# Kernel optimization log

Measured on AMD Instinct MI355X. Metric: run time of the kernel, lower is better.

Reference implementation:

```python
import jax, jax.numpy as jnp
import numpy as np

B, N, D_IN, D_OUT, H, W = 2, 2048, 1024, 1024, 16, 64
DH = D_OUT // H


def setup_inputs() -> dict:
    key = jax.random.key(0)
    ks = jax.random.split(key, 6)
    x = jax.random.normal(ks[0], (B, N, D_IN), dtype=jnp.float32)
    s_in = 1.0 / np.sqrt(D_IN)
    s_out = 1.0 / np.sqrt(D_OUT)
    wq = jax.random.normal(ks[1], (D_IN, D_OUT), dtype=jnp.float32) * s_in
    wk = jax.random.normal(ks[2], (D_IN, D_OUT), dtype=jnp.float32) * s_in
    wv = jax.random.normal(ks[3], (D_IN, D_OUT), dtype=jnp.float32) * s_in
    wo = jax.random.normal(ks[4], (D_OUT, D_OUT), dtype=jnp.float32) * s_out
    # sparse global tokens: every 256th token is global
    global_attention = (jnp.arange(N)[None, :] % 256 == 0) & jnp.ones((B, 1), bool)
    return {"x": x, "wq": wq, "wk": wk, "wv": wv, "wo": wo,
            "global_attention": global_attention}


def _mask(global_attention):
    # True = masked out. Causal local window + global rows/cols unmasked.
    i = jnp.arange(N)[:, None]
    j = jnp.arange(N)[None, :]
    allowed = (i - j < W) & (i >= j)          # causal sliding window
    local_mask = ~allowed                      # [N, N], True = masked
    g = global_attention                       # [B, N] bool
    # global token j clears row j and column j of the mask
    global_clear = g[:, :, None] | g[:, None, :]   # [B, N, N]
    return local_mask[None, :, :] & ~global_clear  # [B, N, N]


def reference(x, wq, wk, wv, wo, global_attention):
    b, n, _ = x.shape
    q = (x @ wq).reshape(b, n, H, DH).transpose(0, 2, 1, 3)  # [b,h,n,dh]
    k = (x @ wk).reshape(b, n, H, DH).transpose(0, 2, 1, 3)
    v = (x @ wv).reshape(b, n, H, DH).transpose(0, 2, 1, 3)
    scores = jnp.einsum('bhqd,bhkd->bhqk', q, k) / jnp.sqrt(jnp.float32(DH))
    mask = _mask(global_attention)[:, None, :, :]            # [b,1,n,n]
    scores = jnp.where(mask, -jnp.inf, scores)
    attn = jax.nn.softmax(scores, axis=-1)
    ctx = jnp.einsum('bhqk,bhkd->bqhd', attn, v).reshape(b, n, D_OUT)
    return ctx @ wo
```

## Files before the change

kernel.cpp:

```cpp
#include <hip/hip_runtime.h>


using u16 = unsigned short;
using u32 = unsigned int;

typedef __attribute__((ext_vector_type(8))) short bf16x8;
typedef __attribute__((ext_vector_type(4))) float f32x4;

__device__ __forceinline__ float b2f(u16 s) {
  union { u32 u; float f; } x; x.u = ((u32)s) << 16; return x.f;
}
__device__ __forceinline__ u16 f2b(float f) {
  union { float f; u32 u; } x; x.f = f;
  u32 r = (x.u + 0x7fffu + ((x.u >> 16) & 1u)) >> 16;
  return (u16)r;
}

__global__ __launch_bounds__(256) void k_pre(const float* __restrict__ x,
                                             u16* __restrict__ xb,
                                             const float* __restrict__ wq,
                                             const float* __restrict__ wk,
                                             const float* __restrict__ wv,
                                             const float* __restrict__ wo,
                                             u16* __restrict__ wqkvT,
                                             u16* __restrict__ woT) {
  __shared__ float tile[64][65];
  const int bid = blockIdx.x;
  if (bid < 2048) {
    int idx = (bid * 256 + threadIdx.x) * 8;
    float4 a = *(const float4*)(x + idx);
    float4 b = *(const float4*)(x + idx + 4);
    uint4 o;
    o.x = (u32)f2b(a.x) | ((u32)f2b(a.y) << 16);
    o.y = (u32)f2b(a.z) | ((u32)f2b(a.w) << 16);
    o.z = (u32)f2b(b.x) | ((u32)f2b(b.y) << 16);
    o.w = (u32)f2b(b.z) | ((u32)f2b(b.w) << 16);
    *(uint4*)(xb + idx) = o;
  } else {
    const int id = bid - 2048;
    const int z = id >> 8, xy = id & 255;
    const float* src = (z == 0) ? wq : (z == 1) ? wk : (z == 2) ? wv : wo;
    u16* dst = (z < 3) ? (wqkvT + ((size_t)z << 20)) : woT;
    const int n0 = (xy & 15) * 64, k0 = (xy >> 4) * 64;
    const int tx = threadIdx.x & 63, ty = threadIdx.x >> 6;
    #pragma unroll
    for (int r = 0; r < 64; r += 4)
      tile[r + ty][tx] = src[(size_t)(k0 + r + ty) * 1024 + n0 + tx];
    __syncthreads();
    #pragma unroll
    for (int r = 0; r < 64; r += 4)
      dst[(size_t)(n0 + r + ty) * 1024 + k0 + tx] = f2b(tile[tx][r + ty]);
  }
}

__device__ __forceinline__ void gload16(const u16* g, u16* l) {
  __builtin_amdgcn_global_load_lds((const __attribute__((address_space(1))) void*)g,
                                   (__attribute__((address_space(3))) void*)l, 16, 0, 0);
}

__global__ __launch_bounds__(512, 4) void k_qkv(const u16* __restrict__ A,
                                                const u16* __restrict__ Bt,
                                                u16* __restrict__ C) {
  __shared__ __attribute__((aligned(16))) u16 lds[40960];
  const int K = 1024, N = 3072, NT = 16;
  const int t = threadIdx.x;
  const int wid = t >> 6, lane = t & 63;
  const int l4 = lane >> 4, l16 = lane & 15;
  const int qr = wid >> 1, qc = wid & 1;
  const int d = blockIdx.y * gridDim.x + blockIdx.x;
  const int qq = (gridDim.x * gridDim.y) >> 3;
  const int tau = (d & 7) * qq + (d >> 3);
  const int bn = tau % gridDim.x, bm = tau / gridDim.x;
  const u16* Ab = A + (size_t)bm * 128 * K;
  const u16* Bb = Bt + (size_t)bn * 192 * K;
  const int rowbase = wid * 8 + (lane >> 3);
  const int qcg = rowbase >> 5, rrb = rowbase & 31;
  const int scc = ((lane & 7) ^ ((lane >> 3) & 7)) << 3;
  const int rsw = (l16 & 7);
  f32x4 acc[3][2][2] = {};
  bf16x8 af[2][2], bf[2][2];

  #define STG_A(BUF, KT)                                                           \
    { u16* lb = lds + (BUF) * 8192 + (wid << 9);                                   \
      _Pragma("unroll")                                                            \
      for (int i = 0; i < 2; ++i)                                                  \
        gload16(Ab + (size_t)(i * 64 + rowbase) * K + (KT) * 64 + scc,             \
                lb + i * 4096); }

  #define STG_B1(BUF, KT, I)                                                       \
    { u16* lb = lds + 16384 + (BUF) * 12288 + (I) * 4096 + (wid << 9);             \
      gload16(Bb + (size_t)(qcg * 96 + (I) * 32 + rrb) * K + (KT) * 64 + scc, lb); }

  #define LOAD_A(AS)                                                               \
    { _Pragma("unroll")                                                            \
      for (int m = 0; m < 2; ++m) {                                                \
        const int ro = qr * 32 + m * 16 + l16;                                     \
        _Pragma("unroll")                                                          \
        for (int ks = 0; ks < 2; ++ks)                                             \
          af[m][ks] = *(const bf16x8*)&(AS)[ro * 64 + (((ks * 4 + l4) ^ rsw) << 3)]; \
      } }

  #define LOAD_B(BS, NH)                                                           \
    { _Pragma("unroll")                                                            \
      for (int n = 0; n < 2; ++n) {                                                \
        const int po = (NH) * 64 + qc * 32 + n * 16 + l16;                         \
        _Pragma("unroll")                                                          \
        for (int ks = 0; ks < 2; ++ks)                                             \
          bf[n][ks] = *(const bf16x8*)&(BS)[po * 64 + (((ks * 4 + l4) ^ rsw) << 3)]; \
      } }

  #define QUAD(NH)                                                                 \
    { __builtin_amdgcn_s_setprio(1);                                               \
      _Pragma("unroll")                                                            \
      for (int m = 0; m < 2; ++m)                                                  \
        _Pragma("unroll")                                                          \
        for (int n = 0; n < 2; ++n) {                                              \
          f32x4 c = acc[NH][m][n];                                                 \
          c = __builtin_amdgcn_mfma_f32_16x16x32_bf16(af[m][0], bf[n][0], c, 0, 0, 0); \
          c = __builtin_amdgcn_mfma_f32_16x16x32_bf16(af[m][1], bf[n][1], c, 0, 0, 0); \
          acc[NH][m][n] = c;                                                       \
        }                                                                          \
      __builtin_amdgcn_s_setprio(0); }

  STG_A(0, 0);
  STG_B1(0, 0, 0); STG_B1(0, 0, 1); STG_B1(0, 0, 2);
  STG_A(1, 1);
  STG_B1(1, 1, 0);
  asm volatile("s_waitcnt vmcnt(3)" ::: "memory");
  __builtin_amdgcn_s_barrier();

  for (int tt = 0; tt < NT; ++tt) {
    const int beta = tt & 1;
    const u16* As = lds + beta * 8192;
    const u16* Bs = lds + 16384 + beta * 12288;
    LOAD_A(As);
    LOAD_B(Bs, 0);
    if (tt + 1 < NT) STG_B1(beta ^ 1, tt + 1, 1);
    __builtin_amdgcn_s_barrier();
    QUAD(0);
    __builtin_amdgcn_s_barrier();
    LOAD_B(Bs, 1);
    if (tt + 1 < NT) STG_B1(beta ^ 1, tt + 1, 2);
    __builtin_amdgcn_s_barrier();
    QUAD(1);
    __builtin_amdgcn_s_barrier();
    LOAD_B(Bs, 2);
    if (tt + 2 < NT) {
      STG_A(beta, tt + 2);
      STG_B1(beta, tt + 2, 0);
    }
    __builtin_amdgcn_s_barrier();
    QUAD(2);
    if (tt + 2 < NT)      asm volatile("s_waitcnt vmcnt(3)" ::: "memory");
    else if (tt + 1 < NT) asm volatile("s_waitcnt vmcnt(0)" ::: "memory");
    __builtin_amdgcn_s_barrier();
  }
  #undef STG_A
  #undef STG_B1
  #undef LOAD_A
  #undef LOAD_B
  #undef QUAD

  #pragma unroll
  for (int nh = 0; nh < 3; ++nh)
    #pragma unroll
    for (int m = 0; m < 2; ++m) {
      const int row0 = bm * 128 + qr * 32 + m * 16 + l4 * 4;
      #pragma unroll
      for (int n = 0; n < 2; ++n) {
        const int col = bn * 192 + qc * 96 + nh * 32 + n * 16 + l16;
        #pragma unroll
        for (int r = 0; r < 4; ++r)
          C[(size_t)(row0 + r) * N + col] = f2b(acc[nh][m][n][r]);
      }
    }
}

__global__ __launch_bounds__(512, 2) void k_out(const u16* __restrict__ A,
                                                const u16* __restrict__ Bt,
                                                float* __restrict__ C,
                                                const float* __restrict__ gpart,
                                                u16* __restrict__ ctxw) {
  __shared__ __attribute__((aligned(16))) u16 lds[32768];
  const int K = 1024, N = 1024, NT = 16;
  const int t = threadIdx.x;
  const int wid = t >> 6, lane = t & 63;
  const int l4 = lane >> 4, l16 = lane & 15;
  const int qr = wid >> 2, qc = wid & 3;
  const int d = blockIdx.y * gridDim.x + blockIdx.x;
  const int qq = (gridDim.x * gridDim.y) >> 3;
  const int tau = (d & 7) * qq + (d >> 3);
  const int bn = tau % gridDim.x, bm = tau / gridDim.x;
  const u16* Ab = A + (size_t)bm * 128 * K;
  const u16* Bb = Bt + (size_t)bn * 128 * K;
  const int rowbase = wid * 8 + (lane >> 3);
  const int qcg = rowbase >> 4, rrb = rowbase & 15;
  const int scc = ((lane & 7) ^ ((lane >> 3) & 7)) << 3;
  const int rsw = (l16 & 7);
  f32x4 acc[2][4] = {};
  bf16x8 af[4][2], bf[2][2];

  if ((bm & 1) == 0) {
    if (t < 256) {
      const int bb = bm >> 4;
      const int irow = (bm & 15) * 128;
      const int row8 = (bm & 15) >> 1;
      const int h = t >> 4;
      const int d0 = (t & 15) * 4;
      const float* g0 = gpart + ((size_t)(bb * 16 + h) * 32) * 520;
      float o0 = 0.f, o1 = 0.f, o2 = 0.f, o3 = 0.f, ls = 0.f;
      for (int q = 0; q < 32; ++q) {
        const float4 v = *(const float4*)(g0 + q * 520 + row8 * 64 + d0);
        o0 += v.x; o1 += v.y; o2 += v.z; o3 += v.w;
        ls += g0[q * 520 + 512 + row8];
      }
      const float inv = 1.f / ls;
      u16* cw = ctxw + ((size_t)(bb * 2048 + irow)) * 1024 + h * 64 + d0;
      cw[0] = f2b(o0 * inv); cw[1] = f2b(o1 * inv);
      cw[2] = f2b(o2 * inv); cw[3] = f2b(o3 * inv);
    }
    __syncthreads();
  }

  #define OSTG_A(BUF, KT)                                                          \
    { u16* lb = lds + (BUF) * 8192 + (wid << 9);                                   \
      _Pragma("unroll")                                                            \
      for (int i = 0; i < 2; ++i)                                                  \
        gload16(Ab + (size_t)(i * 64 + rowbase) * K + (KT) * 64 + scc,             \
                lb + i * 4096); }

  #define OSTG_B(BUF, KT)                                                          \
    { u16* lb = lds + 16384 + (BUF) * 8192 + (wid << 9);                           \
      _Pragma("unroll")                                                            \
      for (int nf = 0; nf < 2; ++nf)                                               \
        gload16(Bb + (size_t)(qcg * 32 + nf * 16 + rrb) * K + (KT) * 64 + scc,     \
                lb + nf * 4096); }

  #define OLOAD()                                                                  \
    { _Pragma("unroll")                                                            \
      for (int m = 0; m < 4; ++m) {                                                \
        const int ro = qr * 64 + m * 16 + l16;                                     \
        _Pragma("unroll")                                                          \
        for (int ks = 0; ks < 2; ++ks)                                             \
          af[m][ks] = *(const bf16x8*)&As[ro * 64 + (((ks * 4 + l4) ^ rsw) << 3)]; \
      }                                                                            \
      _Pragma("unroll")                                                            \
      for (int nf = 0; nf < 2; ++nf) {                                             \
        const int po = nf * 64 + qc * 16 + l16;                                    \
        _Pragma("unroll")                                                          \
        for (int ks = 0; ks < 2; ++ks)                                             \
          bf[nf][ks] = *(const bf16x8*)&Bs[po * 64 + (((ks * 4 + l4) ^ rsw) << 3)]; \
      } }

  OSTG_A(0, 0); OSTG_B(0, 0);
  OSTG_A(1, 1); OSTG_B(1, 1);
  asm volatile("s_waitcnt vmcnt(4)" ::: "memory");
  __builtin_amdgcn_s_barrier();

  for (int tt = 0; tt < NT; ++tt) {
    const int beta = tt & 1;
    const u16* As = lds + beta * 8192;
    const u16* Bs = lds + 16384 + beta * 8192;
    OLOAD();
    asm volatile("s_waitcnt lgkmcnt(0)" ::: "memory");
    __builtin_amdgcn_s_barrier();
    if (tt + 2 < NT) { OSTG_A(beta, tt + 2); OSTG_B(beta, tt + 2); }
    __builtin_amdgcn_s_setprio(1);
    #pragma unroll
    for (int nf = 0; nf < 2; ++nf)
      #pragma unroll
      for (int m = 0; m < 4; ++m) {
        f32x4 c = acc[nf][m];
        c = __builtin_amdgcn_mfma_f32_16x16x32_bf16(af[m][0], bf[nf][0], c, 0, 0, 0);
        c = __builtin_amdgcn_mfma_f32_16x16x32_bf16(af[m][1], bf[nf][1], c, 0, 0, 0);
        acc[nf][m] = c;
      }
    __builtin_amdgcn_s_setprio(0);
    if (tt + 2 < NT)      asm volatile("s_waitcnt vmcnt(4)" ::: "memory");
    else if (tt + 1 < NT) asm volatile("s_waitcnt vmcnt(0)" ::: "memory");
    __builtin_amdgcn_s_barrier();
  }
  #undef OSTG_A
  #undef OSTG_B
  #undef OLOAD

  #pragma unroll
  for (int nf = 0; nf < 2; ++nf)
    #pragma unroll
    for (int m = 0; m < 4; ++m) {
      const int row0 = bm * 128 + qr * 64 + m * 16 + l4 * 4;
      const int col = bn * 128 + qc * 32 + nf * 16 + l16;
      #pragma unroll
      for (int r = 0; r < 4; ++r)
        C[(size_t)(row0 + r) * N + col] = acc[nf][m][r];
    }
}

__global__ __launch_bounds__(256) void k_attn_tile(const u16* __restrict__ qkv,
                                                   u16* __restrict__ ctx,
                                                   float* __restrict__ gpart) {
  __shared__ u16 buf[26880];
  __shared__ u16 Qgs[16 * 72];
  __shared__ u16 Pgs[16 * 72];
  __shared__ float lred[4][16];
  u16* Qs = buf;
  u16* Ks = buf + 4608;
  u16* Vt = buf + 16128;
  u16* Ps = buf;

  const int t = threadIdx.x, wid = t >> 6, lane = t & 63;
  const int l4 = lane >> 4, l16 = lane & 15;
  const int qt = blockIdx.x, h = blockIdx.y, b = blockIdx.z;
  const int q0 = qt * 64;
  const int kbase = q0 - 64;
  const size_t base = (size_t)b * 2048 * 3072;
  const u16* Qg = qkv + base + h * 64;
  const u16* Kg = qkv + base + 1024 + h * 64;
  const u16* Vg = qkv + base + 2048 + h * 64;

  const int rA = t >> 3;
  const int cA = (t & 7) * 8;

  uint4 qv0 = *(const uint4*)&Qg[(size_t)(q0 + rA) * 3072 + cA];
  uint4 qv1 = *(const uint4*)&Qg[(size_t)(q0 + rA + 32) * 3072 + cA];
  uint4 qgv;
  if (t < 64) qgv = *(const uint4*)&Qg[(size_t)(rA * 256) * 3072 + cA];
  uint4 kv0 = *(const uint4*)&Kg[(size_t)max(kbase + rA, 0) * 3072 + cA];
  uint4 kv1 = *(const uint4*)&Kg[(size_t)max(kbase + rA + 32, 0) * 3072 + cA];
  uint4 kv2 = *(const uint4*)&Kg[(size_t)max(kbase + rA + 64, 0) * 3072 + cA];
  uint4 kv3 = *(const uint4*)&Kg[(size_t)max(kbase + rA + 96, 0) * 3072 + cA];
  uint4 kv4;
  if (t < 64) kv4 = *(const uint4*)&Kg[(size_t)(rA * 256) * 3072 + cA];
  uint4 vv0 = *(const uint4*)&Vg[(size_t)max(kbase + rA, 0) * 3072 + cA];
  uint4 vv1 = *(const uint4*)&Vg[(size_t)max(kbase + rA + 32, 0) * 3072 + cA];
  uint4 vv2 = *(const uint4*)&Vg[(size_t)max(kbase + rA + 64, 0) * 3072 + cA];
  uint4 vv3 = *(const uint4*)&Vg[(size_t)max(kbase + rA + 96, 0) * 3072 + cA];
  uint4 vv4;
  if (t < 64) vv4 = *(const uint4*)&Vg[(size_t)(rA * 256) * 3072 + cA];

  for (int z = t; z < 64 * 24; z += 256) {
    int dd = z / 24, j = 136 + z % 24;
    Vt[dd * 168 + j] = 0;
  }
  if (t >= 64 && t < 128) {
    uint4 zz = {0, 0, 0, 0};
    *(uint4*)&Qgs[rA * 72 + cA] = zz;
  }

  *(uint4*)&Qs[rA * 72 + cA] = qv0;
  *(uint4*)&Qs[(rA + 32) * 72 + cA] = qv1;
  if (t < 64) *(uint4*)&Qgs[rA * 72 + cA] = qgv;
  *(uint4*)&Ks[rA * 72 + cA] = kv0;
  *(uint4*)&Ks[(rA + 32) * 72 + cA] = kv1;
  *(uint4*)&Ks[(rA + 64) * 72 + cA] = kv2;
  *(uint4*)&Ks[(rA + 96) * 72 + cA] = kv3;
  if (t < 64) *(uint4*)&Ks[(rA + 128) * 72 + cA] = kv4;

  #define VW1(DD, VAL, CH_, R7_)                                                   \
    { const int kd_ = (((DD) >> 3) ^ (DD)) & 7;                                    \
      const int chs_ = ((CH_) < 16) ? ((CH_) ^ kd_) : (CH_);                       \
      Vt[(DD) * 168 + chs_ * 8 + (R7_)] = (u16)(VAL); }
  #define VTRANS(VV, RR)                                                           \
    { const int ch_ = (RR) >> 3, r7_ = (RR) & 7;                                   \
      VW1(cA + 0, (VV).x & 0xffffu, ch_, r7_)                                      \
      VW1(cA + 1, (VV).x >> 16,     ch_, r7_)                                      \
      VW1(cA + 2, (VV).y & 0xffffu, ch_, r7_)                                      \
      VW1(cA + 3, (VV).y >> 16,     ch_, r7_)                                      \
      VW1(cA + 4, (VV).z & 0xffffu, ch_, r7_)                                      \
      VW1(cA + 5, (VV).z >> 16,     ch_, r7_)                                      \
      VW1(cA + 6, (VV).w & 0xffffu, ch_, r7_)                                      \
      VW1(cA + 7, (VV).w >> 16,     ch_, r7_) }

  VTRANS(vv0, rA)
  VTRANS(vv1, rA + 32)
  VTRANS(vv2, rA + 64)
  VTRANS(vv3, rA + 96)
  if (t < 64) VTRANS(vv4, rA + 128)
  #undef VW1
  #undef VTRANS
  __syncthreads();

  f32x4 sa[10] = {};
  #pragma unroll
  for (int ks = 0; ks < 2; ++ks) {
    bf16x8 qa = *(const bf16x8*)&Qs[(wid * 16 + l16) * 72 + ks * 32 + l4 * 8];
    #pragma unroll
    for (int n = 0; n < 10; ++n) {
      bf16x8 kb = *(const bf16x8*)&Ks[(n * 16 + l16) * 72 + ks * 32 + l4 * 8];
      sa[n] = __builtin_amdgcn_mfma_f32_16x16x32_bf16(qa, kb, sa[n], 0, 0, 0);
    }
  }

  f32x4 sg = {};
  #pragma unroll
  for (int ks = 0; ks < 2; ++ks) {
    bf16x8 qa = *(const bf16x8*)&Qgs[l16 * 72 + ks * 32 + l4 * 8];
    bf16x8 kb = *(const bf16x8*)&Ks[(64 + wid * 16 + l16) * 72 + ks * 32 + l4 * 8];
    sg = __builtin_amdgcn_mfma_f32_16x16x32_bf16(qa, kb, sg, 0, 0, 0);
  }
  #pragma unroll
  for (int r = 0; r < 4; ++r) {
    float p = __expf(sg[r] * 0.125f);
    sg[r] = p;
    #pragma unroll
    for (int o = 1; o < 16; o <<= 1) p += __shfl_xor(p, o);
    if (l16 == 0) lred[wid][l4 * 4 + r] = p;
  }
  #pragma unroll
  for (int r = 0; r < 4; ++r)
    Pgs[(l4 * 4 + r) * 72 + wid * 16 + l16] = f2b(sg[r]);

  const int qi0 = wid * 16 + l4 * 4;
  #pragma unroll
  for (int n = 0; n < 10; ++n) {
    const int jc = n * 16 + l16;
    #pragma unroll
    for (int r = 0; r < 4; ++r) {
      const int qi = qi0 + r;
      bool allowed;
      if (n < 8) {
        const int kr = kbase + jc;
        allowed = (jc > qi) && (jc <= qi + 64) && (kr >= 0) && ((kr & 255) != 0);
      } else {
        allowed = (jc < 136);
      }
      sa[n][r] = allowed ? sa[n][r] * 0.125f : -1e30f;
    }
  }

  float m[4], l[4];
  #pragma unroll
  for (int r = 0; r < 4; ++r) {
    float mx = sa[0][r];
    #pragma unroll
    for (int n = 1; n < 10; ++n) mx = fmaxf(mx, sa[n][r]);
    #pragma unroll
    for (int o = 1; o < 16; o <<= 1) mx = fmaxf(mx, __shfl_xor(mx, o));
    m[r] = mx;
    l[r] = 0.f;
  }
  #pragma unroll
  for (int n = 0; n < 10; ++n)
    #pragma unroll
    for (int r = 0; r < 4; ++r) {
      float p = __expf(sa[n][r] - m[r]);
      sa[n][r] = p;
      l[r] += p;
    }
  #pragma unroll
  for (int r = 0; r < 4; ++r)
    #pragma unroll
    for (int o = 1; o < 16; o <<= 1) l[r] += __shfl_xor(l[r], o);

  __syncthreads();

  u16* Pw = Ps + wid * (16 * 168);
  #pragma unroll
  for (int n = 0; n < 10; ++n)
    #pragma unroll
    for (int r = 0; r < 4; ++r)
      Pw[(l4 * 4 + r) * 168 + n * 16 + l16] = f2b(sa[n][r]);
  __syncthreads();

  f32x4 o[4] = {};
  #pragma unroll
  for (int ks = 0; ks < 5; ++ks) {
    bf16x8 pa = *(const bf16x8*)&Pw[l16 * 168 + ks * 32 + l4 * 8];
    #pragma unroll
    for (int dt = 0; dt < 4; ++dt) {
      const int dvo = dt * 16 + l16;
      const int kdo = ((dvo >> 3) ^ dvo) & 7;
      const int ch = ks * 4 + l4;
      const int chs = (ch < 16) ? (ch ^ kdo) : ch;
      bf16x8 vb = *(const bf16x8*)&Vt[dvo * 168 + chs * 8];
      o[dt] = __builtin_amdgcn_mfma_f32_16x16x32_bf16(pa, vb, o[dt], 0, 0, 0);
    }
  }

  f32x4 og = {};
  {
    const int dV = wid * 16 + l16;
    const int kdg = ((dV >> 3) ^ dV) & 7;
    #pragma unroll
    for (int ks = 0; ks < 2; ++ks) {
      bf16x8 pa = *(const bf16x8*)&Pgs[l16 * 72 + ks * 32 + l4 * 8];
      const int chs = (8 + ks * 4 + l4) ^ kdg;
      bf16x8 vb = *(const bf16x8*)&Vt[dV * 168 + chs * 8];
      og = __builtin_amdgcn_mfma_f32_16x16x32_bf16(pa, vb, og, 0, 0, 0);
    }
  }
  float* gp = gpart + ((size_t)(b * 16 + h) * 32 + qt) * 520;
  #pragma unroll
  for (int r = 0; r < 4; ++r) {
    int row = l4 * 4 + r;
    if (row < 8) gp[row * 64 + wid * 16 + l16] = og[r];
  }
  if (t < 8) gp[512 + t] = lred[0][t] + lred[1][t] + lred[2][t] + lred[3][t];

  #pragma unroll
  for (int r = 0; r < 4; ++r) {
    const int q = q0 + qi0 + r;
    if ((q & 255) == 0) continue;
    const float inv = 1.0f / l[r];
    #pragma unroll
    for (int dt = 0; dt < 4; ++dt)
      ctx[(size_t)(b * 2048 + q) * 1024 + h * 64 + dt * 16 + l16] = f2b(o[dt][r] * inv);
  }
}

extern "C" void kernel_launch(void* const* d_in, const int* in_sizes, int n_in,
                              void* d_out, int out_size, void* d_ws, size_t ws_size,
                              hipStream_t stream) {
  (void)in_sizes; (void)n_in; (void)out_size; (void)ws_size;
  const float* x  = (const float*)d_in[0];
  const float* wq = (const float*)d_in[1];
  const float* wk = (const float*)d_in[2];
  const float* wv = (const float*)d_in[3];
  const float* wo = (const float*)d_in[4];
  char* ws = (char*)d_ws;
  u16* xb    = (u16*)(ws);
  u16* qkv   = (u16*)(ws + (8u  << 20));
  u16* ctx   = (u16*)(ws + (32u << 20));
  u16* wqkvT = (u16*)(ws + (40u << 20));
  u16* woT   = (u16*)(ws + (46u << 20));
  float* gpart = (float*)(ws);

  k_pre<<<3072, 256, 0, stream>>>(x, xb, wq, wk, wv, wo, wqkvT, woT);
  k_qkv<<<dim3(16, 32), 512, 0, stream>>>(xb, wqkvT, qkv);
  k_attn_tile<<<dim3(32, 16, 2), 256, 0, stream>>>(qkv, ctx, gpart);
  k_out<<<dim3(8, 32), 512, 0, stream>>>(ctx, woT, (float*)d_out, gpart, ctx);
}
```

Measured before the change: 75.40 us.

## Restructure QKV GEMM main loop to load all B fragments before MFMAs

The QKV GEMM k-loop moves from three barrier-separated sub-phases to one phase per k-tile. Each phase loads every A and B fragment from LDS into registers, issues all global-to-LDS prefetches for tile tt+2 at once, then runs all 24 MFMAs under raised priority. This cuts the barriers per iteration from six to two and lets the whole MFMA block run without LDS stalls between quads. The cost is more B fragment registers, so launch bounds drop from 4 to 2 blocks per SM, which may lower occupancy.

Result: slower. 79.71 us (+5.7%).

```diff
diff --git a/kernel.cpp b/kernel.cpp
--- a/kernel.cpp
+++ b/kernel.cpp
@@ -58,7 +58,7 @@
                                    (__attribute__((address_space(3))) void*)l, 16, 0, 0);
 }
 
-__global__ __launch_bounds__(512, 4) void k_qkv(const u16* __restrict__ A,
+__global__ __launch_bounds__(512, 2) void k_qkv(const u16* __restrict__ A,
                                                 const u16* __restrict__ Bt,
                                                 u16* __restrict__ C) {
   __shared__ __attribute__((aligned(16))) u16 lds[40960];
@@ -78,7 +78,7 @@
   const int scc = ((lane & 7) ^ ((lane >> 3) & 7)) << 3;
   const int rsw = (l16 & 7);
   f32x4 acc[3][2][2] = {};
-  bf16x8 af[2][2], bf[2][2];
+  bf16x8 af[2][2], bfl[3][2][2];
 
   #define STG_A(BUF, KT)                                                           \
     { u16* lb = lds + (BUF) * 8192 + (wid << 9);                                   \
@@ -106,27 +106,26 @@
         const int po = (NH) * 64 + qc * 32 + n * 16 + l16;                         \
         _Pragma("unroll")                                                          \
         for (int ks = 0; ks < 2; ++ks)                                             \
-          bf[n][ks] = *(const bf16x8*)&(BS)[po * 64 + (((ks * 4 + l4) ^ rsw) << 3)]; \
+          bfl[NH][n][ks] =                                                         \
+              *(const bf16x8*)&(BS)[po * 64 + (((ks * 4 + l4) ^ rsw) << 3)];       \
       } }
 
   #define QUAD(NH)                                                                 \
-    { __builtin_amdgcn_s_setprio(1);                                               \
-      _Pragma("unroll")                                                            \
+    { _Pragma("unroll")                                                            \
       for (int m = 0; m < 2; ++m)                                                  \
         _Pragma("unroll")                                                          \
         for (int n = 0; n < 2; ++n) {                                              \
           f32x4 c = acc[NH][m][n];                                                 \
-          c = __builtin_amdgcn_mfma_f32_16x16x32_bf16(af[m][0], bf[n][0], c, 0, 0, 0); \
-          c = __builtin_amdgcn_mfma_f32_16x16x32_bf16(af[m][1], bf[n][1], c, 0, 0, 0); \
+          c = __builtin_amdgcn_mfma_f32_16x16x32_bf16(af[m][0], bfl[NH][n][0],     \
+                                                      c, 0, 0, 0);                 \
+          c = __builtin_amdgcn_mfma_f32_16x16x32_bf16(af[m][1], bfl[NH][n][1],     \
+                                                      c, 0, 0, 0);                 \
           acc[NH][m][n] = c;                                                       \
-        }                                                                          \
-      __builtin_amdgcn_s_setprio(0); }
-
-  STG_A(0, 0);
-  STG_B1(0, 0, 0); STG_B1(0, 0, 1); STG_B1(0, 0, 2);
-  STG_A(1, 1);
-  STG_B1(1, 1, 0);
-  asm volatile("s_waitcnt vmcnt(3)" ::: "memory");
+        } }
+
+  STG_A(0, 0); STG_B1(0, 0, 0); STG_B1(0, 0, 1); STG_B1(0, 0, 2);
+  STG_A(1, 1); STG_B1(1, 1, 0); STG_B1(1, 1, 1); STG_B1(1, 1, 2);
+  asm volatile("s_waitcnt vmcnt(5)" ::: "memory");
   __builtin_amdgcn_s_barrier();
 
   for (int tt = 0; tt < NT; ++tt) {
@@ -135,23 +134,20 @@
     const u16* Bs = lds + 16384 + beta * 12288;
     LOAD_A(As);
     LOAD_B(Bs, 0);
-    if (tt + 1 < NT) STG_B1(beta ^ 1, tt + 1, 1);
+    LOAD_B(Bs, 1);
+    LOAD_B(Bs, 2);
+    asm volatile("s_waitcnt lgkmcnt(0)" ::: "memory");
     __builtin_amdgcn_s_barrier();
-    QUAD(0);
-    __builtin_amdgcn_s_barrier();
-    LOAD_B(Bs, 1);
-    if (tt + 1 < NT) STG_B1(beta ^ 1, tt + 1, 2);
-    __builtin_amdgcn_s_barrier();
-    QUAD(1);
-    __builtin_amdgcn_s_barrier();
-    LOAD_B(Bs, 2);
     if (tt + 2 < NT) {
       STG_A(beta, tt + 2);
-      STG_B1(beta, tt + 2, 0);
-    }
-    __builtin_amdgcn_s_barrier();
+      STG_B1(beta, tt + 2, 0); STG_B1(beta, tt + 2, 1); STG_B1(beta, tt + 2, 2);
+    }
+    __builtin_amdgcn_s_setprio(1);
+    QUAD(0);
+    QUAD(1);
     QUAD(2);
-    if (tt + 2 < NT)      asm volatile("s_waitcnt vmcnt(3)" ::: "memory");
+    __builtin_amdgcn_s_setprio(0);
+    if (tt + 2 < NT)      asm volatile("s_waitcnt vmcnt(5)" ::: "memory");
     else if (tt + 1 < NT) asm volatile("s_waitcnt vmcnt(0)" ::: "memory");
     __builtin_amdgcn_s_barrier();
   }
```
